# Performance work log

Measured on AMD Instinct MI355X. Metric: run time of the kernel, lower is better.

## Reference

```python
import jax, jax.numpy as jnp
import numpy as np

NUM_HEADS = 16


def _rope(x, c, s):
    # x: [T, H, D]; c, s: [T, D/2] -> rotate-half RoPE over full head_dim
    d2 = c.shape[-1]
    x1, x2 = x[..., :d2], x[..., d2:]
    c = c[:, None, :]
    s = s[:, None, :]
    return jnp.concatenate([x1 * c - x2 * s, x2 * c + x1 * s], axis=-1)


def setup_inputs() -> dict:
    key = jax.random.key(0)
    ks = jax.random.split(key, 4)
    B, L, dim = 8, 1024, 1024
    T = B * L
    D = dim // NUM_HEADS
    hidden_states = jax.random.normal(ks[0], (T, dim), dtype=jnp.float32)
    w_qkv = jax.random.normal(ks[1], (dim, 3 * dim), dtype=jnp.float32) * (dim ** -0.5)
    b_qkv = jnp.zeros((3 * dim,), dtype=jnp.float32)
    w_proj = jax.random.normal(ks[2], (dim, dim), dtype=jnp.float32) * (dim ** -0.5)
    b_proj = jnp.zeros((dim,), dtype=jnp.float32)
    # RoPE tables: positions restart at 0 for each packed sequence
    pos = jnp.tile(jnp.arange(L, dtype=jnp.float32), B)  # [T]
    inv_freq = 1.0 / (10000.0 ** (jnp.arange(0, D, 2, dtype=jnp.float32) / D))  # [D/2]
    freqs = pos[:, None] * inv_freq[None, :]  # [T, D/2]
    emb = jnp.concatenate([freqs, freqs], axis=-1)  # [T, D]
    cos = jnp.cos(emb)
    sin = jnp.sin(emb)
    cu_seqlens = (jnp.arange(B + 1, dtype=jnp.int32) * L)
    return {"hidden_states": hidden_states, "cos": cos, "sin": sin,
            "w_qkv": w_qkv, "b_qkv": b_qkv, "w_proj": w_proj, "b_proj": b_proj,
            "cu_seqlens": cu_seqlens}


def reference(hidden_states, cos, sin, w_qkv, b_qkv, w_proj, b_proj, cu_seqlens):
    T, dim = hidden_states.shape
    H = NUM_HEADS
    D = dim // H
    B = cu_seqlens.shape[0] - 1  # equal-length packed sequences
    L = T // B

    qkv = hidden_states @ w_qkv + b_qkv            # [T, 3*dim]
    qkv = qkv.reshape(T, 3, H, D)
    q, k, v = qkv[:, 0], qkv[:, 1], qkv[:, 2]       # [T, H, D]

    # module chunks cos/sin in half along last dim before apply_rotary_emb
    c = cos[..., : D // 2].astype(jnp.float32)
    s = sin[..., : D // 2].astype(jnp.float32)
    q = _rope(q.astype(jnp.float32), c, s).astype(hidden_states.dtype)
    k = _rope(k.astype(jnp.float32), c, s).astype(hidden_states.dtype)

    # varlen flash attention == block-diagonal attention; equal lengths -> reshape
    qb = q.reshape(B, L, H, D)
    kb = k.reshape(B, L, H, D)
    vb = v.reshape(B, L, H, D)
    scale = D ** -0.5
    scores = jnp.einsum("bqhd,bkhd->bhqk", qb, kb) * scale  # [B, H, L, L]
    probs = jax.nn.softmax(scores, axis=-1)
    out = jnp.einsum("bhqk,bkhd->bqhd", probs, vb)           # [B, L, H, D]
    out = out.reshape(T, dim)
    return out @ w_proj + b_proj
```

## Files before the change

kernel.cpp:

```cpp
#include <hip/hip_runtime.h>

typedef unsigned short ushort_t;
typedef __attribute__((ext_vector_type(8))) short short8;
typedef __attribute__((ext_vector_type(4))) float f32x4;

#define AS1 __attribute__((address_space(1)))
#define AS3 __attribute__((address_space(3)))

__device__ __forceinline__ ushort_t f2bf(float f) {
  unsigned int u = __builtin_bit_cast(unsigned int, f);
  u += 0x7fffu + ((u >> 16) & 1u);
  return (ushort_t)(u >> 16);
}

__device__ __forceinline__ unsigned int pack_bf2(float a, float b) {
  unsigned int ua = __builtin_bit_cast(unsigned int, a) + 0x8000u;
  unsigned int ub = __builtin_bit_cast(unsigned int, b) + 0x8000u;
  return (ua >> 16) | (ub & 0xffff0000u);
}

__device__ __forceinline__ void load_lds16(const ushort_t* g, ushort_t* l) {
  __builtin_amdgcn_global_load_lds((AS1 void*)g, (AS3 void*)l, 16, 0, 0);
}

#define MFMA16(a, b, c) __builtin_amdgcn_mfma_f32_16x16x32_bf16((a), (b), (c), 0, 0, 0)

__global__ __launch_bounds__(256) void k_convert(const float* __restrict__ src,
                                                 ushort_t* __restrict__ dst, int n8) {
  int i = blockIdx.x * 256 + threadIdx.x;
  if (i >= n8) return;
  const float4* s4 = (const float4*)src;
  float4 a = s4[(size_t)i * 2], b = s4[(size_t)i * 2 + 1];
  short8 o;
  o[0] = (short)f2bf(a.x); o[1] = (short)f2bf(a.y);
  o[2] = (short)f2bf(a.z); o[3] = (short)f2bf(a.w);
  o[4] = (short)f2bf(b.x); o[5] = (short)f2bf(b.y);
  o[6] = (short)f2bf(b.z); o[7] = (short)f2bf(b.w);
  *(short8*)(dst + (size_t)i * 8) = o;
}

__global__ __launch_bounds__(256) void k_transpose_bf16(const float* __restrict__ src,
                                                        ushort_t* __restrict__ dst,
                                                        int R, int C) {
  __shared__ ushort_t t[64 * 65];
  const int x0 = blockIdx.x * 64, y0 = blockIdx.y * 64;
  const int c = threadIdx.x & 63, r0 = threadIdx.x >> 6;
#pragma unroll
  for (int i = 0; i < 16; ++i) {
    int r = r0 + i * 4;
    t[c * 65 + r] = f2bf(src[(size_t)(y0 + r) * C + x0 + c]);
  }
  __syncthreads();
#pragma unroll
  for (int i = 0; i < 16; ++i) {
    int rr = r0 + i * 4;
    dst[(size_t)(x0 + rr) * R + y0 + c] = t[rr * 65 + c];
  }
}

__global__ __launch_bounds__(256) void k_qkv_gemm_rope(
    const ushort_t* __restrict__ A, const ushort_t* __restrict__ Bt,
    const float* __restrict__ bias, const float* __restrict__ cosb,
    const float* __restrict__ sinb, ushort_t* __restrict__ Qb,
    ushort_t* __restrict__ Kb, ushort_t* __restrict__ Vb) {
  constexpr int K = 1024;
  __shared__ __align__(16) ushort_t As[128 * 64];
  __shared__ __align__(16) ushort_t Bs[128 * 64];
  const int tid = threadIdx.x, lane = tid & 63, wave = tid >> 6;
  const int quad = lane >> 4, ml = lane & 15;
  const int wm = wave & 1, wn = wave >> 1;
  const int m0 = blockIdx.y * 128, n0 = blockIdx.x * 128;
  f32x4 acc[4][4] = {};

  for (int kt = 0; kt < K / 64; ++kt) {
    __syncthreads();
    {
      const int kk0 = kt * 64;
#pragma unroll
      for (int i = 0; i < 4; ++i) {
        int cch = i * 256 + tid;
        int r = cch >> 3, s = cch & 7, gs = s ^ (r & 7);
        load_lds16(A + (size_t)(m0 + r) * K + kk0 + gs * 8, As + cch * 8);
        load_lds16(Bt + (size_t)(n0 + r) * K + kk0 + gs * 8, Bs + cch * 8);
      }
    }
    __syncthreads();
#pragma unroll
    for (int ks = 0; ks < 2; ++ks) {
      short8 af[4], bfr[4];
#pragma unroll
      for (int mb = 0; mb < 4; ++mb) {
        int row = wm * 64 + mb * 16 + ml;
        int gs = (ks * 4 + quad) ^ (row & 7);
        af[mb] = *(const short8*)(As + row * 64 + gs * 8);
      }
#pragma unroll
      for (int nb = 0; nb < 4; ++nb) {
        int row = wn * 64 + nb * 16 + ml;
        int gs = (ks * 4 + quad) ^ (row & 7);
        bfr[nb] = *(const short8*)(Bs + row * 64 + gs * 8);
      }
#pragma unroll
      for (int mb = 0; mb < 4; ++mb)
#pragma unroll
        for (int nb = 0; nb < 4; ++nb)
          acc[mb][nb] = MFMA16(af[mb], bfr[nb], acc[mb][nb]);
    }
  }

  const int ncol0 = n0 + wn * 64;
  const int sec = ncol0 >> 10;
  const int h = (ncol0 & 1023) >> 6;
#pragma unroll
  for (int mb = 0; mb < 4; ++mb) {
#pragma unroll
    for (int rg = 0; rg < 4; ++rg) {
      const int m = m0 + wm * 64 + mb * 16 + quad * 4 + rg;
      const int b = m >> 10, l = m & 1023;
      const size_t ob = ((size_t)(b * 16 + h) * 1024 + l) * 64;
      if (sec < 2) {
        ushort_t* dst = (sec == 0) ? Qb : Kb;
#pragma unroll
        for (int nb = 0; nb < 2; ++nb) {
          const int d = nb * 16 + ml;
          float x1 = acc[mb][nb][rg] + bias[ncol0 + d];
          float x2 = acc[mb][nb + 2][rg] + bias[ncol0 + d + 32];
          float cv = cosb[(size_t)m * 64 + d];
          float sv = sinb[(size_t)m * 64 + d];
          dst[ob + d] = f2bf(x1 * cv - x2 * sv);
          dst[ob + d + 32] = f2bf(x2 * cv + x1 * sv);
        }
      } else {
#pragma unroll
        for (int nb = 0; nb < 4; ++nb) {
          const int d = nb * 16 + ml;
          Vb[ob + d] = f2bf(acc[mb][nb][rg] + bias[ncol0 + d]);
        }
      }
    }
  }
}

__global__ __launch_bounds__(256, 4) void k_attn(const ushort_t* __restrict__ Qb,
                                                 const ushort_t* __restrict__ Kb,
                                                 const ushort_t* __restrict__ Vb,
                                                 ushort_t* __restrict__ Ob) {
  __shared__ __align__(16) ushort_t QP[9216];
  __shared__ __align__(16) ushort_t Ks[64 * 64];
  __shared__ __align__(16) ushort_t Vts[64 * 72];
  const int tid = threadIdx.x, lane = tid & 63, wave = tid >> 6;
  const int quad = lane >> 4, ml = lane & 15;
  const int bh = blockIdx.x & 127, qt = blockIdx.x >> 7;
  const int q0 = qt * 128;
  const size_t base = (size_t)bh * (1024 * 64);
  const float CEXP = 0.18033688011112042f;

#pragma unroll
  for (int i = 0; i < 4; ++i) {
    int cch = i * 256 + tid;
    int r = cch >> 3, s = cch & 7, gs = s ^ (r & 7);
    load_lds16(Qb + base + (size_t)(q0 + r) * 64 + gs * 8, QP + cch * 8);
  }
  __syncthreads();

  short8 qf[2][2];
#pragma unroll
  for (int mb = 0; mb < 2; ++mb)
#pragma unroll
    for (int ks = 0; ks < 2; ++ks) {
      int row = wave * 32 + mb * 16 + ml;
      int gs = (ks * 4 + quad) ^ (row & 7);
      qf[mb][ks] = *(const short8*)(QP + row * 64 + gs * 8);
    }

  ushort_t* Pw = QP + wave * 2304;
  f32x4 Oacc[2][4] = {};
  float lsum[2][4] = {};

  for (int kt = 0; kt < 16; ++kt) {
    __syncthreads();
#pragma unroll
    for (int i = 0; i < 2; ++i) {
      int cch = i * 256 + tid;
      int r = cch >> 3, s = cch & 7, gs = s ^ (r & 7);
      load_lds16(Kb + base + (size_t)(kt * 64 + r) * 64 + gs * 8, Ks + cch * 8);
    }
    {
      const int k = tid & 63, d0 = (tid >> 6) * 16;
      const int c = (k & 15) * 4 + (k >> 4);
      const ushort_t* g = Vb + base + (size_t)(kt * 64 + k) * 64 + d0;
      short8 v0 = *(const short8*)g;
      short8 v1 = *(const short8*)(g + 8);
#pragma unroll
      for (int j = 0; j < 8; ++j) Vts[(d0 + j) * 72 + c] = (ushort_t)v0[j];
#pragma unroll
      for (int j = 0; j < 8; ++j) Vts[(d0 + 8 + j) * 72 + c] = (ushort_t)v1[j];
    }
    __syncthreads();

    f32x4 Sacc[2][4] = {};
#pragma unroll
    for (int nb = 0; nb < 4; ++nb)
#pragma unroll
      for (int ks = 0; ks < 2; ++ks) {
        int row = nb * 16 + ml;
        int gs = (ks * 4 + quad) ^ (row & 7);
        short8 kf = *(const short8*)(Ks + row * 64 + gs * 8);
        Sacc[0][nb] = MFMA16(qf[0][ks], kf, Sacc[0][nb]);
        Sacc[1][nb] = MFMA16(qf[1][ks], kf, Sacc[1][nb]);
      }

#pragma unroll
    for (int mb = 0; mb < 2; ++mb) {
#pragma unroll
      for (int rg = 0; rg < 4; ++rg) {
        float p0 = exp2f(Sacc[mb][0][rg] * CEXP);
        float p1 = exp2f(Sacc[mb][1][rg] * CEXP);
        float p2 = exp2f(Sacc[mb][2][rg] * CEXP);
        float p3 = exp2f(Sacc[mb][3][rg] * CEXP);
        lsum[mb][rg] += (p0 + p1) + (p2 + p3);
        uint2 w;
        w.x = pack_bf2(p0, p1);
        w.y = pack_bf2(p2, p3);
        *(uint2*)(Pw + (mb * 16 + quad * 4 + rg) * 72 + ml * 4) = w;
      }
    }

#pragma unroll
    for (int ks = 0; ks < 2; ++ks) {
      short8 pf[2];
#pragma unroll
      for (int mb = 0; mb < 2; ++mb)
        pf[mb] = *(const short8*)(Pw + (mb * 16 + ml) * 72 + ks * 32 + quad * 8);
#pragma unroll
      for (int nb = 0; nb < 4; ++nb) {
        short8 vf = *(const short8*)(Vts + (nb * 16 + ml) * 72 + ks * 32 + quad * 8);
        Oacc[0][nb] = MFMA16(pf[0], vf, Oacc[0][nb]);
        Oacc[1][nb] = MFMA16(pf[1], vf, Oacc[1][nb]);
      }
    }
  }

  const int b = bh >> 4, h = bh & 15;
#pragma unroll
  for (int mb = 0; mb < 2; ++mb) {
#pragma unroll
    for (int rg = 0; rg < 4; ++rg) {
      float l = lsum[mb][rg];
      l += __shfl_xor(l, 1);
      l += __shfl_xor(l, 2);
      l += __shfl_xor(l, 4);
      l += __shfl_xor(l, 8);
      float inv = 1.f / l;
      int q = q0 + wave * 32 + mb * 16 + quad * 4 + rg;
      size_t ob = ((size_t)(b * 1024 + q)) * 1024 + h * 64;
#pragma unroll
      for (int nb = 0; nb < 4; ++nb)
        Ob[ob + nb * 16 + ml] = f2bf(Oacc[mb][nb][rg] * inv);
    }
  }
}

__global__ __launch_bounds__(256) void k_proj_gemm(const ushort_t* __restrict__ A,
                                                   const ushort_t* __restrict__ Bt,
                                                   const float* __restrict__ bias,
                                                   float* __restrict__ out) {
  constexpr int K = 1024;
  __shared__ __align__(16) ushort_t As[128 * 32];
  __shared__ __align__(16) ushort_t Bs[128 * 32];
  const int tid = threadIdx.x, lane = tid & 63, wave = tid >> 6;
  const int quad = lane >> 4, ml = lane & 15;
  const int wm = wave & 1, wn = wave >> 1;
  const int m0 = blockIdx.y * 128, n0 = blockIdx.x * 128;
  f32x4 acc[4][4] = {};

  for (int kt = 0; kt < K / 32; ++kt) {
    __syncthreads();
    {
      const int kk0 = kt * 32;
#pragma unroll
      for (int i = 0; i < 2; ++i) {
        int cch = i * 256 + tid;
        int r = cch >> 2, s = cch & 3, gs = s ^ ((r >> 1) & 3);
        load_lds16(A + (size_t)(m0 + r) * K + kk0 + gs * 8, As + cch * 8);
        load_lds16(Bt + (size_t)(n0 + r) * K + kk0 + gs * 8, Bs + cch * 8);
      }
    }
    __syncthreads();
    short8 af[4], bfr[4];
#pragma unroll
    for (int mb = 0; mb < 4; ++mb) {
      int row = wm * 64 + mb * 16 + ml;
      int seg = quad ^ ((row >> 1) & 3);
      af[mb] = *(const short8*)(As + row * 32 + seg * 8);
    }
#pragma unroll
    for (int nb = 0; nb < 4; ++nb) {
      int row = wn * 64 + nb * 16 + ml;
      int seg = quad ^ ((row >> 1) & 3);
      bfr[nb] = *(const short8*)(Bs + row * 32 + seg * 8);
    }
#pragma unroll
    for (int mb = 0; mb < 4; ++mb)
#pragma unroll
      for (int nb = 0; nb < 4; ++nb)
        acc[mb][nb] = MFMA16(af[mb], bfr[nb], acc[mb][nb]);
  }
#pragma unroll
  for (int mb = 0; mb < 4; ++mb) {
#pragma unroll
    for (int rg = 0; rg < 4; ++rg) {
      const int m = m0 + wm * 64 + mb * 16 + quad * 4 + rg;
#pragma unroll
      for (int nb = 0; nb < 4; ++nb) {
        const int n = n0 + wn * 64 + nb * 16 + ml;
        out[(size_t)m * 1024 + n] = acc[mb][nb][rg] + bias[n];
      }
    }
  }
}

extern "C" void kernel_launch(void* const* d_in, const int* in_sizes, int n_in,
                              void* d_out, int out_size, void* d_ws, size_t ws_size,
                              hipStream_t stream) {
  const float* hs = (const float*)d_in[0];
  const float* cosb = (const float*)d_in[1];
  const float* sinb = (const float*)d_in[2];
  const float* wqkv = (const float*)d_in[3];
  const float* bqkv = (const float*)d_in[4];
  const float* wproj = (const float*)d_in[5];
  const float* bproj = (const float*)d_in[6];
  float* out = (float*)d_out;

  char* ws = (char*)d_ws;
  ushort_t* hsb = (ushort_t*)(ws);
  ushort_t* wqkvT = (ushort_t*)(ws + (16u << 20));
  ushort_t* wprojT = (ushort_t*)(ws + (22u << 20));
  ushort_t* Qb = (ushort_t*)(ws + (24u << 20));
  ushort_t* Kb = (ushort_t*)(ws + (40u << 20));
  ushort_t* Vb = (ushort_t*)(ws + (56u << 20));
  ushort_t* attnb = hsb;

  k_convert<<<4096, 256, 0, stream>>>(hs, hsb, 1048576);
  k_transpose_bf16<<<dim3(48, 16), 256, 0, stream>>>(wqkv, wqkvT, 1024, 3072);
  k_transpose_bf16<<<dim3(16, 16), 256, 0, stream>>>(wproj, wprojT, 1024, 1024);
  k_qkv_gemm_rope<<<dim3(24, 64), 256, 0, stream>>>(hsb, wqkvT, bqkv, cosb, sinb,
                                                    Qb, Kb, Vb);
  k_attn<<<1024, 256, 0, stream>>>(Qb, Kb, Vb, attnb);
  k_proj_gemm<<<dim3(8, 64), 256, 0, stream>>>(attnb, wprojT, bproj, out);
}
```

Before: 286.9 us.

## Merge weight transposes, enlarge QKV GEMM M-tile, deepen proj GEMM K-tile

```diff
diff --git a/kernel.cpp b/kernel.cpp
--- a/kernel.cpp
+++ b/kernel.cpp
@@ -39,11 +39,18 @@
   *(short8*)(dst + (size_t)i * 8) = o;
 }
 
-__global__ __launch_bounds__(256) void k_transpose_bf16(const float* __restrict__ src,
-                                                        ushort_t* __restrict__ dst,
-                                                        int R, int C) {
+__global__ __launch_bounds__(256) void k_transpose_w(const float* __restrict__ wqkv,
+                                                     ushort_t* __restrict__ wqkvT,
+                                                     const float* __restrict__ wproj,
+                                                     ushort_t* __restrict__ wprojT) {
   __shared__ ushort_t t[64 * 65];
-  const int x0 = blockIdx.x * 64, y0 = blockIdx.y * 64;
+  const float* src;
+  ushort_t* dst;
+  int C, bx;
+  if (blockIdx.x < 48) { src = wqkv; dst = wqkvT; C = 3072; bx = blockIdx.x; }
+  else { src = wproj; dst = wprojT; C = 1024; bx = blockIdx.x - 48; }
+  const int R = 1024;
+  const int x0 = bx * 64, y0 = blockIdx.y * 64;
   const int c = threadIdx.x & 63, r0 = threadIdx.x >> 6;
 #pragma unroll
   for (int i = 0; i < 16; ++i) {
@@ -58,18 +65,18 @@
   }
 }
 
-__global__ __launch_bounds__(256) void k_qkv_gemm_rope(
+__global__ __launch_bounds__(512) void k_qkv_gemm_rope(
     const ushort_t* __restrict__ A, const ushort_t* __restrict__ Bt,
     const float* __restrict__ bias, const float* __restrict__ cosb,
     const float* __restrict__ sinb, ushort_t* __restrict__ Qb,
     ushort_t* __restrict__ Kb, ushort_t* __restrict__ Vb) {
   constexpr int K = 1024;
-  __shared__ __align__(16) ushort_t As[128 * 64];
+  __shared__ __align__(16) ushort_t As[256 * 64];
   __shared__ __align__(16) ushort_t Bs[128 * 64];
   const int tid = threadIdx.x, lane = tid & 63, wave = tid >> 6;
   const int quad = lane >> 4, ml = lane & 15;
-  const int wm = wave & 1, wn = wave >> 1;
-  const int m0 = blockIdx.y * 128, n0 = blockIdx.x * 128;
+  const int wm = wave & 3, wn = wave >> 2;
+  const int m0 = blockIdx.y * 256, n0 = blockIdx.x * 128;
   f32x4 acc[4][4] = {};
 
   for (int kt = 0; kt < K / 64; ++kt) {
@@ -78,9 +85,14 @@
       const int kk0 = kt * 64;
 #pragma unroll
       for (int i = 0; i < 4; ++i) {
-        int cch = i * 256 + tid;
+        int cch = i * 512 + tid;
         int r = cch >> 3, s = cch & 7, gs = s ^ (r & 7);
         load_lds16(A + (size_t)(m0 + r) * K + kk0 + gs * 8, As + cch * 8);
+      }
+#pragma unroll
+      for (int i = 0; i < 2; ++i) {
+        int cch = i * 512 + tid;
+        int r = cch >> 3, s = cch & 7, gs = s ^ (r & 7);
         load_lds16(Bt + (size_t)(n0 + r) * K + kk0 + gs * 8, Bs + cch * 8);
       }
     }
@@ -266,45 +278,48 @@
                                                    const float* __restrict__ bias,
                                                    float* __restrict__ out) {
   constexpr int K = 1024;
-  __shared__ __align__(16) ushort_t As[128 * 32];
-  __shared__ __align__(16) ushort_t Bs[128 * 32];
+  __shared__ __align__(16) ushort_t As[128 * 64];
+  __shared__ __align__(16) ushort_t Bs[128 * 64];
   const int tid = threadIdx.x, lane = tid & 63, wave = tid >> 6;
   const int quad = lane >> 4, ml = lane & 15;
   const int wm = wave & 1, wn = wave >> 1;
   const int m0 = blockIdx.y * 128, n0 = blockIdx.x * 128;
   f32x4 acc[4][4] = {};
 
-  for (int kt = 0; kt < K / 32; ++kt) {
+  for (int kt = 0; kt < K / 64; ++kt) {
     __syncthreads();
     {
-      const int kk0 = kt * 32;
-#pragma unroll
-      for (int i = 0; i < 2; ++i) {
+      const int kk0 = kt * 64;
+#pragma unroll
+      for (int i = 0; i < 4; ++i) {
         int cch = i * 256 + tid;
-        int r = cch >> 2, s = cch & 3, gs = s ^ ((r >> 1) & 3);
+        int r = cch >> 3, s = cch & 7, gs = s ^ (r & 7);
         load_lds16(A + (size_t)(m0 + r) * K + kk0 + gs * 8, As + cch * 8);
         load_lds16(Bt + (size_t)(n0 + r) * K + kk0 + gs * 8, Bs + cch * 8);
       }
     }
     __syncthreads();
-    short8 af[4], bfr[4];
-#pragma unroll
-    for (int mb = 0; mb < 4; ++mb) {
-      int row = wm * 64 + mb * 16 + ml;
-      int seg = quad ^ ((row >> 1) & 3);
-      af[mb] = *(const short8*)(As + row * 32 + seg * 8);
-    }
-#pragma unroll
-    for (int nb = 0; nb < 4; ++nb) {
-      int row = wn * 64 + nb * 16 + ml;
-      int seg = quad ^ ((row >> 1) & 3);
-      bfr[nb] = *(const short8*)(Bs + row * 32 + seg * 8);
-    }
-#pragma unroll
-    for (int mb = 0; mb < 4; ++mb)
-#pragma unroll
-      for (int nb = 0; nb < 4; ++nb)
-        acc[mb][nb] = MFMA16(af[mb], bfr[nb], acc[mb][nb]);
+#pragma unroll
+    for (int ks = 0; ks < 2; ++ks) {
+      short8 af[4], bfr[4];
+#pragma unroll
+      for (int mb = 0; mb < 4; ++mb) {
+        int row = wm * 64 + mb * 16 + ml;
+        int gs = (ks * 4 + quad) ^ (row & 7);
+        af[mb] = *(const short8*)(As + row * 64 + gs * 8);
+      }
+#pragma unroll
+      for (int nb = 0; nb < 4; ++nb) {
+        int row = wn * 64 + nb * 16 + ml;
+        int gs = (ks * 4 + quad) ^ (row & 7);
+        bfr[nb] = *(const short8*)(Bs + row * 64 + gs * 8);
+      }
+#pragma unroll
+      for (int mb = 0; mb < 4; ++mb)
+#pragma unroll
+        for (int nb = 0; nb < 4; ++nb)
+          acc[mb][nb] = MFMA16(af[mb], bfr[nb], acc[mb][nb]);
+    }
   }
 #pragma unroll
   for (int mb = 0; mb < 4; ++mb) {
@@ -342,9 +357,8 @@
   ushort_t* attnb = hsb;
 
   k_convert<<<4096, 256, 0, stream>>>(hs, hsb, 1048576);
-  k_transpose_bf16<<<dim3(48, 16), 256, 0, stream>>>(wqkv, wqkvT, 1024, 3072);
-  k_transpose_bf16<<<dim3(16, 16), 256, 0, stream>>>(wproj, wprojT, 1024, 1024);
-  k_qkv_gemm_rope<<<dim3(24, 64), 256, 0, stream>>>(hsb, wqkvT, bqkv, cosb, sinb,
+  k_transpose_w<<<dim3(64, 16), 256, 0, stream>>>(wqkv, wqkvT, wproj, wprojT);
+  k_qkv_gemm_rope<<<dim3(24, 32), 512, 0, stream>>>(hsb, wqkvT, bqkv, cosb, sinb,
                                                     Qb, Kb, Vb);
   k_attn<<<1024, 256, 0, stream>>>(Qb, Kb, Vb, attnb);
   k_proj_gemm<<<dim3(8, 64), 256, 0, stream>>>(attnb, wprojT, bproj, out);
```

Result: faster. 265.6 us (-7.4%).
